# Kernel optimization log

Hardware: AMD Instinct MI355X
Metric: run time of the kernel (lower is better)

## Reference

```python
import jax, jax.numpy as jnp
import numpy as np

LN_EPS = 1e-3  # keras LayerNormalization default epsilon


def setup_inputs() -> dict:
    key = jax.random.key(0)
    k1, k2, k3 = jax.random.split(key, 3)
    B, N, D, F = 512, 1000, 128, 2
    H = jax.random.normal(k1, (B, N, D), dtype=jnp.float32)
    indice = jax.random.randint(k2, (B, F), 0, N, dtype=jnp.int32)
    # Dense: (F+1)*D -> D (graph context adds one row before flatten)
    W = jax.random.normal(k3, ((F + 1) * D, D), dtype=jnp.float32) * (1.0 / np.sqrt((F + 1) * D))
    b = jnp.zeros((D,), dtype=jnp.float32)
    gamma = jnp.ones((D,), dtype=jnp.float32)
    beta = jnp.zeros((D,), dtype=jnp.float32)
    return {"H": H, "indice": indice, "W": W, "b": b, "gamma": gamma, "beta": beta}


def reference(H, indice, W, b, gamma, beta):
    B, N, D = H.shape
    # _indice_embedding: one-hot expand+tile+reduce == direct gather H[b, indice[b,f]]
    indice_emb = jnp.take_along_axis(H, indice[..., None].astype(jnp.int32), axis=1)  # (B, F, D)
    graph_emb = jnp.mean(H, axis=1, keepdims=True)  # (B, 1, D)
    emb = jnp.concatenate([indice_emb, graph_emb], axis=1).reshape(B, -1)  # (B, (F+1)*D)
    x = jax.nn.relu(emb @ W + b)  # (B, D)
    mean = jnp.mean(x, axis=-1, keepdims=True)
    var = jnp.var(x, axis=-1, keepdims=True)
    x = gamma * (x - mean) * jax.lax.rsqrt(var + LN_EPS) + beta
    return x[:, None, :]  # (B, 1, D)
```

## Files before the change

kernel.cpp:

```cpp
#include <hip/hip_runtime.h>

constexpr int B = 512;
constexpr int N = 1000;
constexpr int D = 128;
constexpr int F = 2;
constexpr float LN_EPS = 1e-3f;

__global__ __launch_bounds__(1024) void fused_gather_mean_dense_ln(
    const float* __restrict__ H, const int* __restrict__ indice,
    const float* __restrict__ W, const float* __restrict__ bias,
    const float* __restrict__ gamma, const float* __restrict__ beta,
    float* __restrict__ out)
{
    const int b   = blockIdx.x;
    const int tid = threadIdx.x;
    const float* __restrict__ Hb = H + (size_t)b * (N * D);

    __shared__ float  semb[(F + 1) * D];
    __shared__ float4 spart[32][32];

    const int c4 = tid & 31;
    const int rg = tid >> 5;
    float4 acc = make_float4(0.f, 0.f, 0.f, 0.f);
    #pragma unroll 4
    for (int n = rg; n < N; n += 32) {
        const float4 v = *reinterpret_cast<const float4*>(Hb + n * D + c4 * 4);
        acc.x += v.x; acc.y += v.y; acc.z += v.z; acc.w += v.w;
    }
    spart[rg][c4] = acc;

    if (tid < 64) {
        const int f   = tid >> 5;
        const int idx = indice[b * F + f];
        const float4 v = *reinterpret_cast<const float4*>(Hb + idx * D + c4 * 4);
        *reinterpret_cast<float4*>(&semb[f * D + c4 * 4]) = v;
    }
    __syncthreads();

    if (tid < 32) {
        float4 s = spart[0][tid];
        #pragma unroll
        for (int g = 1; g < 32; ++g) {
            const float4 p = spart[g][tid];
            s.x += p.x; s.y += p.y; s.z += p.z; s.w += p.w;
        }
        const float inv = 1.0f / (float)N;
        *reinterpret_cast<float4*>(&semb[2 * D + tid * 4]) =
            make_float4(s.x * inv, s.y * inv, s.z * inv, s.w * inv);
    }
    __syncthreads();

    if (tid < 32) {
        const float4* __restrict__ W4 = reinterpret_cast<const float4*>(W);
        float4 x = reinterpret_cast<const float4*>(bias)[tid];
        for (int k = 0; k < (F + 1) * D; ++k) {
            const float  e = semb[k];
            const float4 w = W4[k * 32 + tid];
            x.x = fmaf(e, w.x, x.x);
            x.y = fmaf(e, w.y, x.y);
            x.z = fmaf(e, w.z, x.z);
            x.w = fmaf(e, w.w, x.w);
        }
        x.x = fmaxf(x.x, 0.f); x.y = fmaxf(x.y, 0.f);
        x.z = fmaxf(x.z, 0.f); x.w = fmaxf(x.w, 0.f);

        float s  = x.x + x.y + x.z + x.w;
        float s2 = x.x * x.x + x.y * x.y + x.z * x.z + x.w * x.w;
        #pragma unroll
        for (int off = 1; off < 32; off <<= 1) {
            s  += __shfl_xor(s,  off);
            s2 += __shfl_xor(s2, off);
        }
        const float mean = s  * (1.0f / (float)D);
        const float var  = s2 * (1.0f / (float)D) - mean * mean;
        const float rstd = rsqrtf(var + LN_EPS);

        const float4 g4 = reinterpret_cast<const float4*>(gamma)[tid];
        const float4 b4 = reinterpret_cast<const float4*>(beta)[tid];
        float4 y;
        y.x = g4.x * (x.x - mean) * rstd + b4.x;
        y.y = g4.y * (x.y - mean) * rstd + b4.y;
        y.z = g4.z * (x.z - mean) * rstd + b4.z;
        y.w = g4.w * (x.w - mean) * rstd + b4.w;
        reinterpret_cast<float4*>(out)[b * 32 + tid] = y;
    }
}

extern "C" void kernel_launch(void* const* d_in, const int* in_sizes, int n_in,
                              void* d_out, int out_size, void* d_ws, size_t ws_size,
                              hipStream_t stream) {
    const float* H      = (const float*)d_in[0];
    const int*   indice = (const int*)  d_in[1];
    const float* W      = (const float*)d_in[2];
    const float* bias   = (const float*)d_in[3];
    const float* gamma  = (const float*)d_in[4];
    const float* beta   = (const float*)d_in[5];
    float* out = (float*)d_out;

    fused_gather_mean_dense_ln<<<dim3(B), dim3(1024), 0, stream>>>(
        H, indice, W, bias, gamma, beta, out);
}
```

Measured before the change: 55.47 us.

## Split column-sum into chunked kernel and parallelize dense+layernorm across threads

Moves the per-batch mean over H into a separate kernel with four row chunks per batch and smaller 256-thread blocks using nontemporal loads, writing partial sums to workspace. A second kernel combines the partials, gathers the indexed rows, and computes the dense layer with one output per thread before a two-wave LayerNorm reduction. This removes the serialized 32-lane dense tail from the bandwidth-bound block and raises parallelism, at the cost of an extra launch and workspace round-trip.

```diff
diff --git a/kernel.cpp b/kernel.cpp
--- a/kernel.cpp
+++ b/kernel.cpp
@@ -6,84 +6,95 @@
 constexpr int F = 2;
 constexpr float LN_EPS = 1e-3f;
 
-__global__ __launch_bounds__(1024) void fused_gather_mean_dense_ln(
-    const float* __restrict__ H, const int* __restrict__ indice,
-    const float* __restrict__ W, const float* __restrict__ bias,
-    const float* __restrict__ gamma, const float* __restrict__ beta,
-    float* __restrict__ out)
+constexpr int CHUNKS = 4;
+constexpr int ROWS_PER_CHUNK = N / CHUNKS;
+
+typedef float fx4 __attribute__((ext_vector_type(4)));
+
+__global__ __launch_bounds__(256) void colsum_kernel(
+    const float* __restrict__ H, fx4* __restrict__ ws)
 {
-    const int b   = blockIdx.x;
+    const int blk = blockIdx.x;
+    const int b   = blk >> 2;
+    const int ch  = blk & 3;
     const int tid = threadIdx.x;
+    const int c4  = tid & 31;
+    const int rg  = tid >> 5;
+
     const float* __restrict__ Hb = H + (size_t)b * (N * D);
+    const int nstart = ch * ROWS_PER_CHUNK;
+    const int nend   = nstart + ROWS_PER_CHUNK;
 
-    __shared__ float  semb[(F + 1) * D];
-    __shared__ float4 spart[32][32];
+    fx4 acc = (fx4)(0.f);
+    #pragma unroll 4
+    for (int n = nstart + rg; n < nend; n += 8) {
+        const fx4 v = __builtin_nontemporal_load(
+            reinterpret_cast<const fx4*>(Hb + n * D + c4 * 4));
+        acc += v;
+    }
 
-    const int c4 = tid & 31;
-    const int rg = tid >> 5;
-    float4 acc = make_float4(0.f, 0.f, 0.f, 0.f);
-    #pragma unroll 4
-    for (int n = rg; n < N; n += 32) {
-        const float4 v = *reinterpret_cast<const float4*>(Hb + n * D + c4 * 4);
-        acc.x += v.x; acc.y += v.y; acc.z += v.z; acc.w += v.w;
-    }
-    spart[rg][c4] = acc;
-
-    if (tid < 64) {
-        const int f   = tid >> 5;
-        const int idx = indice[b * F + f];
-        const float4 v = *reinterpret_cast<const float4*>(Hb + idx * D + c4 * 4);
-        *reinterpret_cast<float4*>(&semb[f * D + c4 * 4]) = v;
-    }
+    __shared__ fx4 sp[8][32];
+    sp[rg][c4] = acc;
     __syncthreads();
 
     if (tid < 32) {
-        float4 s = spart[0][tid];
+        fx4 s = sp[0][tid];
         #pragma unroll
-        for (int g = 1; g < 32; ++g) {
-            const float4 p = spart[g][tid];
-            s.x += p.x; s.y += p.y; s.z += p.z; s.w += p.w;
-        }
-        const float inv = 1.0f / (float)N;
-        *reinterpret_cast<float4*>(&semb[2 * D + tid * 4]) =
-            make_float4(s.x * inv, s.y * inv, s.z * inv, s.w * inv);
+        for (int g = 1; g < 8; ++g) s += sp[g][tid];
+        ws[(size_t)(b * CHUNKS + ch) * 32 + tid] = s;
     }
+}
+
+__global__ __launch_bounds__(128) void gather_dense_ln(
+    const float* __restrict__ H, const int* __restrict__ indice,
+    const float* __restrict__ ws, const float* __restrict__ W,
+    const float* __restrict__ bias, const float* __restrict__ gamma,
+    const float* __restrict__ beta, float* __restrict__ out)
+{
+    const int b = blockIdx.x;
+    const int o = threadIdx.x;
+
+    __shared__ float semb[(F + 1) * D];
+    __shared__ float sred[2], sred2[2];
+
+    const float* __restrict__ Hb = H + (size_t)b * (N * D);
+    const int i0 = indice[b * F + 0];
+    const int i1 = indice[b * F + 1];
+    semb[o]       = Hb[i0 * D + o];
+    semb[D + o]   = Hb[i1 * D + o];
+    const float cs = ws[(size_t)(b * CHUNKS + 0) * D + o]
+                   + ws[(size_t)(b * CHUNKS + 1) * D + o]
+                   + ws[(size_t)(b * CHUNKS + 2) * D + o]
+                   + ws[(size_t)(b * CHUNKS + 3) * D + o];
+    semb[2 * D + o] = cs * (1.0f / (float)N);
     __syncthreads();
 
-    if (tid < 32) {
-        const float4* __restrict__ W4 = reinterpret_cast<const float4*>(W);
-        float4 x = reinterpret_cast<const float4*>(bias)[tid];
-        for (int k = 0; k < (F + 1) * D; ++k) {
-            const float  e = semb[k];
-            const float4 w = W4[k * 32 + tid];
-            x.x = fmaf(e, w.x, x.x);
-            x.y = fmaf(e, w.y, x.y);
-            x.z = fmaf(e, w.z, x.z);
-            x.w = fmaf(e, w.w, x.w);
-        }
-        x.x = fmaxf(x.x, 0.f); x.y = fmaxf(x.y, 0.f);
-        x.z = fmaxf(x.z, 0.f); x.w = fmaxf(x.w, 0.f);
+    float x0 = bias[o], x1 = 0.f, x2 = 0.f, x3 = 0.f;
+    #pragma unroll 8
+    for (int k = 0; k < (F + 1) * D; k += 4) {
+        x0 = fmaf(semb[k + 0], W[(k + 0) * D + o], x0);
+        x1 = fmaf(semb[k + 1], W[(k + 1) * D + o], x1);
+        x2 = fmaf(semb[k + 2], W[(k + 2) * D + o], x2);
+        x3 = fmaf(semb[k + 3], W[(k + 3) * D + o], x3);
+    }
+    float x = fmaxf((x0 + x1) + (x2 + x3), 0.f);
 
-        float s  = x.x + x.y + x.z + x.w;
-        float s2 = x.x * x.x + x.y * x.y + x.z * x.z + x.w * x.w;
-        #pragma unroll
-        for (int off = 1; off < 32; off <<= 1) {
-            s  += __shfl_xor(s,  off);
-            s2 += __shfl_xor(s2, off);
-        }
-        const float mean = s  * (1.0f / (float)D);
-        const float var  = s2 * (1.0f / (float)D) - mean * mean;
-        const float rstd = rsqrtf(var + LN_EPS);
+    float s = x, s2 = x * x;
+    #pragma unroll
+    for (int off = 1; off < 64; off <<= 1) {
+        s  += __shfl_xor(s,  off);
+        s2 += __shfl_xor(s2, off);
+    }
+    const int wid = o >> 6;
+    if ((o & 63) == 0) { sred[wid] = s; sred2[wid] = s2; }
+    __syncthreads();
+    const float S  = sred[0]  + sred[1];
+    const float S2 = sred2[0] + sred2[1];
+    const float mean = S * (1.0f / (float)D);
+    const float var  = S2 * (1.0f / (float)D) - mean * mean;
+    const float rstd = rsqrtf(var + LN_EPS);
 
-        const float4 g4 = reinterpret_cast<const float4*>(gamma)[tid];
-        const float4 b4 = reinterpret_cast<const float4*>(beta)[tid];
-        float4 y;
-        y.x = g4.x * (x.x - mean) * rstd + b4.x;
-        y.y = g4.y * (x.y - mean) * rstd + b4.y;
-        y.z = g4.z * (x.z - mean) * rstd + b4.z;
-        y.w = g4.w * (x.w - mean) * rstd + b4.w;
-        reinterpret_cast<float4*>(out)[b * 32 + tid] = y;
-    }
+    out[(size_t)b * D + o] = gamma[o] * (x - mean) * rstd + beta[o];
 }
 
 extern "C" void kernel_launch(void* const* d_in, const int* in_sizes, int n_in,
@@ -96,7 +107,10 @@
     const float* gamma  = (const float*)d_in[4];
     const float* beta   = (const float*)d_in[5];
     float* out = (float*)d_out;
+    float* ws  = (float*)d_ws;
 
-    fused_gather_mean_dense_ln<<<dim3(B), dim3(1024), 0, stream>>>(
-        H, indice, W, bias, gamma, beta, out);
+    colsum_kernel<<<dim3(B * CHUNKS), dim3(256), 0, stream>>>(
+        H, reinterpret_cast<fx4*>(ws));
+    gather_dense_ln<<<dim3(B), dim3(128), 0, stream>>>(
+        H, indice, ws, W, bias, gamma, beta, out);
 }
```

After: 50.83 us. -8.4%, faster.

## Split column-sum into multi-block kernel and parallelize dense layer across warps

Applied to the files above, without the earlier changes.

The single fused kernel becomes two. A column-sum kernel splits each batch's 1000 rows across 8 (or 4) blocks and writes partial sums to workspace. A second kernel gathers the indexed rows, reduces the partials, and spreads the 384x128 matvec across 8 warps with split-K and a shared-memory reduction. Batches from index 448 onward use nontemporal loads, apparently to keep the earlier batches' H rows resident in cache for the gather. This adds a second launch and a workspace round trip in exchange for many more blocks streaming H and a much shorter serial matvec.

```diff
diff --git a/kernel.cpp b/kernel.cpp
--- a/kernel.cpp
+++ b/kernel.cpp
@@ -6,61 +6,100 @@
 constexpr int F = 2;
 constexpr float LN_EPS = 1e-3f;
 
-__global__ __launch_bounds__(1024) void fused_gather_mean_dense_ln(
+constexpr int NT_SPLIT = 448;
+
+typedef float fx4 __attribute__((ext_vector_type(4)));
+
+template<int CH>
+__global__ __launch_bounds__(256) void colsum_kernel(
+    const float* __restrict__ H, fx4* __restrict__ ws)
+{
+    constexpr int RPC = N / CH;
+    const int blk = blockIdx.x;
+    const int b   = blk / CH;
+    const int ch  = blk % CH;
+    const int tid = threadIdx.x;
+    const int c4  = tid & 31;
+    const int rg  = tid >> 5;
+
+    const float* __restrict__ Hb = H + (size_t)b * (N * D);
+    const int nstart = ch * RPC;
+    const int nend   = nstart + RPC;
+
+    fx4 acc = (fx4)(0.f);
+    if (b < NT_SPLIT) {
+        #pragma unroll 8
+        for (int n = nstart + rg; n < nend; n += 8)
+            acc += *reinterpret_cast<const fx4*>(Hb + (size_t)n * D + c4 * 4);
+    } else {
+        #pragma unroll 8
+        for (int n = nstart + rg; n < nend; n += 8)
+            acc += __builtin_nontemporal_load(
+                reinterpret_cast<const fx4*>(Hb + (size_t)n * D + c4 * 4));
+    }
+
+    __shared__ fx4 sp[8][32];
+    sp[rg][c4] = acc;
+    __syncthreads();
+
+    if (tid < 32) {
+        fx4 s = sp[0][tid];
+        #pragma unroll
+        for (int g = 1; g < 8; ++g) s += sp[g][tid];
+        ws[(size_t)(b * CH + ch) * 32 + tid] = s;
+    }
+}
+
+template<int CH>
+__global__ __launch_bounds__(256) void gather_dense_ln(
     const float* __restrict__ H, const int* __restrict__ indice,
-    const float* __restrict__ W, const float* __restrict__ bias,
-    const float* __restrict__ gamma, const float* __restrict__ beta,
-    float* __restrict__ out)
+    const float* __restrict__ ws, const float* __restrict__ W,
+    const float* __restrict__ bias, const float* __restrict__ gamma,
+    const float* __restrict__ beta, float* __restrict__ out)
 {
     const int b   = blockIdx.x;
     const int tid = threadIdx.x;
     const float* __restrict__ Hb = H + (size_t)b * (N * D);
 
-    __shared__ float  semb[(F + 1) * D];
-    __shared__ float4 spart[32][32];
+    __shared__ float semb[(F + 1) * D];
+    __shared__ fx4 sx[8][32];
 
-    const int c4 = tid & 31;
-    const int rg = tid >> 5;
-    float4 acc = make_float4(0.f, 0.f, 0.f, 0.f);
-    #pragma unroll 4
-    for (int n = rg; n < N; n += 32) {
-        const float4 v = *reinterpret_cast<const float4*>(Hb + n * D + c4 * 4);
-        acc.x += v.x; acc.y += v.y; acc.z += v.z; acc.w += v.w;
+    {
+        const int f   = tid >> 7;
+        const int col = tid & 127;
+        const int idx = indice[b * F + f];
+        semb[f * D + col] = Hb[(size_t)idx * D + col];
     }
-    spart[rg][c4] = acc;
+    if (tid < 128) {
+        float cs = 0.f;
+        #pragma unroll
+        for (int g = 0; g < CH; ++g)
+            cs += reinterpret_cast<const float*>(ws)[(size_t)(b * CH + g) * D + tid];
+        semb[2 * D + tid] = cs * (1.0f / (float)N);
+    }
+    __syncthreads();
 
-    if (tid < 64) {
-        const int f   = tid >> 5;
-        const int idx = indice[b * F + f];
-        const float4 v = *reinterpret_cast<const float4*>(Hb + idx * D + c4 * 4);
-        *reinterpret_cast<float4*>(&semb[f * D + c4 * 4]) = v;
+    {
+        const int ksl = tid >> 5;
+        const int c4  = tid & 31;
+        const fx4* __restrict__ W4 = reinterpret_cast<const fx4*>(W);
+        fx4 a0 = (fx4)(0.f), a1 = (fx4)(0.f), a2 = (fx4)(0.f), a3 = (fx4)(0.f);
+        const int k0 = ksl * 48;
+        #pragma unroll 4
+        for (int k = k0; k < k0 + 48; k += 4) {
+            a0 += semb[k + 0] * W4[(size_t)(k + 0) * 32 + c4];
+            a1 += semb[k + 1] * W4[(size_t)(k + 1) * 32 + c4];
+            a2 += semb[k + 2] * W4[(size_t)(k + 2) * 32 + c4];
+            a3 += semb[k + 3] * W4[(size_t)(k + 3) * 32 + c4];
+        }
+        sx[ksl][c4] = (a0 + a1) + (a2 + a3);
     }
     __syncthreads();
 
     if (tid < 32) {
-        float4 s = spart[0][tid];
+        fx4 x = reinterpret_cast<const fx4*>(bias)[tid];
         #pragma unroll
-        for (int g = 1; g < 32; ++g) {
-            const float4 p = spart[g][tid];
-            s.x += p.x; s.y += p.y; s.z += p.z; s.w += p.w;
-        }
-        const float inv = 1.0f / (float)N;
-        *reinterpret_cast<float4*>(&semb[2 * D + tid * 4]) =
-            make_float4(s.x * inv, s.y * inv, s.z * inv, s.w * inv);
-    }
-    __syncthreads();
-
-    if (tid < 32) {
-        const float4* __restrict__ W4 = reinterpret_cast<const float4*>(W);
-        float4 x = reinterpret_cast<const float4*>(bias)[tid];
-        for (int k = 0; k < (F + 1) * D; ++k) {
-            const float  e = semb[k];
-            const float4 w = W4[k * 32 + tid];
-            x.x = fmaf(e, w.x, x.x);
-            x.y = fmaf(e, w.y, x.y);
-            x.z = fmaf(e, w.z, x.z);
-            x.w = fmaf(e, w.w, x.w);
-        }
+        for (int g = 0; g < 8; ++g) x += sx[g][tid];
         x.x = fmaxf(x.x, 0.f); x.y = fmaxf(x.y, 0.f);
         x.z = fmaxf(x.z, 0.f); x.w = fmaxf(x.w, 0.f);
 
@@ -75,14 +114,14 @@
         const float var  = s2 * (1.0f / (float)D) - mean * mean;
         const float rstd = rsqrtf(var + LN_EPS);
 
-        const float4 g4 = reinterpret_cast<const float4*>(gamma)[tid];
-        const float4 b4 = reinterpret_cast<const float4*>(beta)[tid];
-        float4 y;
+        const fx4 g4 = reinterpret_cast<const fx4*>(gamma)[tid];
+        const fx4 b4 = reinterpret_cast<const fx4*>(beta)[tid];
+        fx4 y;
         y.x = g4.x * (x.x - mean) * rstd + b4.x;
         y.y = g4.y * (x.y - mean) * rstd + b4.y;
         y.z = g4.z * (x.z - mean) * rstd + b4.z;
         y.w = g4.w * (x.w - mean) * rstd + b4.w;
-        reinterpret_cast<float4*>(out)[b * 32 + tid] = y;
+        reinterpret_cast<fx4*>(out)[(size_t)b * 32 + tid] = y;
     }
 }
 
@@ -96,7 +135,16 @@
     const float* gamma  = (const float*)d_in[4];
     const float* beta   = (const float*)d_in[5];
     float* out = (float*)d_out;
+    fx4*   ws  = (fx4*)d_ws;
 
-    fused_gather_mean_dense_ln<<<dim3(B), dim3(1024), 0, stream>>>(
-        H, indice, W, bias, gamma, beta, out);
+    const size_t need8 = (size_t)B * 8 * D * sizeof(float);
+    if (ws_size >= need8) {
+        colsum_kernel<8><<<dim3(B * 8), dim3(256), 0, stream>>>(H, ws);
+        gather_dense_ln<8><<<dim3(B), dim3(256), 0, stream>>>(
+            H, indice, (const float*)ws, W, bias, gamma, beta, out);
+    } else {
+        colsum_kernel<4><<<dim3(B * 4), dim3(256), 0, stream>>>(H, ws);
+        gather_dense_ln<4><<<dim3(B), dim3(256), 0, stream>>>(
+            H, indice, (const float*)ws, W, bias, gamma, beta, out);
+    }
 }
```

Measured after the change: 53.71 us. -3.2%, faster.
